# Kernel tuning notes

Hardware: AMD Instinct MI355X
Metric: run time of the kernel (lower is better)

## Reference

```python
import jax, jax.numpy as jnp
import numpy as np

EPS = 1e-5
NH, NP = 12, 4  # heads, points per level


def _ln(x, g, b):
    m = x.mean(-1, keepdims=True)
    v = x.var(-1, keepdims=True)
    return (x - m) / jnp.sqrt(v + EPS) * g + b


def _bilinear(v, g, H_, W_):
    # v: [B, nh, H_*W_, d] flattened feature map; g: [B, nh, Lq, np, 2] normalized locs in [0,1]
    # torch grid_sample(align_corners=False, padding='zeros') with grid = 2*loc-1 => pixel = loc*W - 0.5
    x = g[..., 0] * W_ - 0.5
    y = g[..., 1] * H_ - 0.5
    x0 = jnp.floor(x)
    y0 = jnp.floor(y)
    wx1 = x - x0
    wy1 = y - y0
    wx0 = 1.0 - wx1
    wy0 = 1.0 - wy1
    d = v.shape[-1]
    Bn, nh, Lq, np_ = x.shape
    out = jnp.zeros((Bn, nh, Lq, np_, d), v.dtype)
    for xi, yi, w in ((x0, y0, wx0 * wy0), (x0 + 1, y0, wx1 * wy0),
                      (x0, y0 + 1, wx0 * wy1), (x0 + 1, y0 + 1, wx1 * wy1)):
        valid = (xi >= 0) & (xi < W_) & (yi >= 0) & (yi < H_)
        xc = jnp.clip(xi, 0, W_ - 1).astype(jnp.int32)
        yc = jnp.clip(yi, 0, H_ - 1).astype(jnp.int32)
        idx = (yc * W_ + xc).reshape(Bn, nh, Lq * np_, 1)
        gv = jnp.take_along_axis(v, idx, axis=2).reshape(Bn, nh, Lq, np_, d)
        out = out + (w * valid.astype(v.dtype))[..., None] * gv
    return out


def setup_inputs() -> dict:
    key = jax.random.key(0)
    ks = jax.random.split(key, 16)
    B, Lq, C = 4, 4096, 768
    nl = 1
    Hs = Ws = 64
    Lin = Hs * Ws
    hid = int(C * 0.25)
    s = 0.02
    f32 = jnp.float32
    return {
        'query': jax.random.normal(ks[0], (B, Lq, C), f32),
        'reference_points': jax.random.uniform(ks[1], (B, Lq, nl, 2), f32),
        'feat': jax.random.normal(ks[2], (B, Lin, C), f32),
        'spatial_shapes': np.array([[Hs, Ws]], dtype=np.int64),
        'level_start_index': np.array([0], dtype=np.int64),
        'H': Hs, 'W': Ws,
        'qn_g': jnp.ones(C, f32), 'qn_b': jnp.zeros(C, f32),
        'fn_g': jnp.ones(C, f32), 'fn_b': jnp.zeros(C, f32),
        'Wv': jax.random.normal(ks[3], (C, C), f32) * s, 'bv': jnp.zeros(C, f32),
        'Woff': jax.random.normal(ks[4], (C, NH * nl * NP * 2), f32) * s,
        'boff': jax.random.normal(ks[5], (NH * nl * NP * 2,), f32) * 0.1,
        'Watt': jax.random.normal(ks[6], (C, NH * nl * NP), f32) * s,
        'batt': jnp.zeros(NH * nl * NP, f32),
        'Wout': jax.random.normal(ks[7], (C, C), f32) * s, 'bout': jnp.zeros(C, f32),
        'ffn_g': jnp.ones(C, f32), 'ffn_b': jnp.zeros(C, f32),
        'W1': jax.random.normal(ks[8], (C, hid), f32) * s, 'b1': jnp.zeros(hid, f32),
        'W2': jax.random.normal(ks[9], (hid, C), f32) * s, 'b2': jnp.zeros(C, f32),
    }


def reference(query, reference_points, feat, spatial_shapes, level_start_index, H, W,
              qn_g, qn_b, fn_g, fn_b, Wv, bv, Woff, boff, Watt, batt, Wout, bout,
              ffn_g, ffn_b, W1, b1, W2, b2):
    B, Lq, C = query.shape
    nl = spatial_shapes.shape[0]
    d = C // NH
    qn = _ln(query, qn_g, qn_b)
    fn = _ln(feat, fn_g, fn_b)
    value = (fn @ Wv + bv).reshape(B, -1, NH, d)
    off = (qn @ Woff + boff).reshape(B, Lq, NH, nl, NP, 2)
    attw = jax.nn.softmax((qn @ Watt + batt).reshape(B, Lq, NH, nl * NP), axis=-1)
    attw = attw.reshape(B, Lq, NH, nl, NP)
    # offset normalizer is [W_l, H_l]
    norm = np.stack([spatial_shapes[:, 1], spatial_shapes[:, 0]], -1).astype(np.float32)
    loc = reference_points[:, :, None, :, None, :] + off / jnp.asarray(norm)[None, None, None, :, None, :]
    out = jnp.zeros((B, NH, Lq, d), query.dtype)
    for l in range(nl):
        H_, W_ = int(spatial_shapes[l, 0]), int(spatial_shapes[l, 1])
        s0 = int(level_start_index[l])
        v = value[:, s0:s0 + H_ * W_].transpose(0, 2, 1, 3)       # [B, nh, HW, d]
        g = loc[:, :, :, l].transpose(0, 2, 1, 3, 4)              # [B, nh, Lq, np, 2]
        sampled = _bilinear(v, g, H_, W_)                         # [B, nh, Lq, np, d]
        w = attw[:, :, :, l].transpose(0, 2, 1, 3)                # [B, nh, Lq, np]
        out = out + jnp.sum(sampled * w[..., None], axis=3)
    attn = out.transpose(0, 2, 1, 3).reshape(B, Lq, C) @ Wout + bout
    query = query + attn
    h = _ln(query, ffn_g, ffn_b)
    h = jax.nn.gelu(h @ W1 + b1, approximate=False)
    return query + (h @ W2 + b2)
```

## Files before the change

kernel.cpp:

```cpp
#include <hip/hip_runtime.h>
#include <hip/hip_bf16.h>
#include <math.h>

#define B_    4
#define LQ    4096
#define CC    768
#define NH_   12
#define DH    64
#define NP_   4
#define HH    64
#define WW    64
#define HID   192
#define ROWS  (B_ * LQ)
#define EPS_  1e-5f

typedef __bf16 bf16x8 __attribute__((ext_vector_type(8)));
typedef __bf16 bf16x4 __attribute__((ext_vector_type(4)));
typedef float  f32x4  __attribute__((ext_vector_type(4)));

typedef __attribute__((address_space(3))) void* lds_vp;
typedef const __attribute__((address_space(1))) void* gbl_vp;

__device__ __forceinline__ unsigned pk4_f8(float a, float b, float c, float d) {
    unsigned lo, hi;
    asm volatile("v_cvt_pk_fp8_f32 %0, %1, %2" : "=v"(lo) : "v"(a), "v"(b));
    asm volatile("v_cvt_pk_fp8_f32 %0, %1, %2" : "=v"(hi) : "v"(c), "v"(d));
    return (lo & 0xffffu) | (hi << 16);
}
__device__ __forceinline__ unsigned char to_f8(float a) {
    unsigned r;
    asm volatile("v_cvt_pk_fp8_f32 %0, %1, %1" : "=v"(r) : "v"(a));
    return (unsigned char)r;
}

struct PrepJob { const float* W; unsigned char* Wt; int K; int N; int Npad; };
struct PrepJobs { PrepJob j[6]; };

__inline__ __device__ float wave_sum64(float v) {
    #pragma unroll
    for (int o = 32; o > 0; o >>= 1) v += __shfl_down(v, o, 64);
    return v;
}

__global__ __launch_bounds__(256)
void ln2p_kernel(const float* __restrict__ x0, const float* __restrict__ g0,
                 const float* __restrict__ b0, unsigned char* __restrict__ y0,
                 const float* __restrict__ x1, const float* __restrict__ g1,
                 const float* __restrict__ b1, unsigned char* __restrict__ y1,
                 PrepJobs jobs) {
    __shared__ float tile[64][65];
    __shared__ float red[8];
    int bx = blockIdx.x;
    int t = threadIdx.x;

    if (bx >= 2 * ROWS) {
        int tid = bx - 2 * ROWS;
        PrepJob job = jobs.j[tid / 144];
        int rem = tid % 144;
        int k0 = (rem % 12) * 64, n0 = (rem / 12) * 64;
        if (k0 >= job.K || n0 >= job.Npad) return;
        int c = t & 63, r0 = t >> 6;
        #pragma unroll
        for (int i = 0; i < 16; ++i) {
            int kk = i * 4 + r0;
            float v = 0.f;
            if (k0 + kk < job.K && n0 + c < job.N) v = job.W[(size_t)(k0 + kk) * job.N + n0 + c];
            tile[kk][c] = v;
        }
        __syncthreads();
        #pragma unroll
        for (int i = 0; i < 16; ++i) {
            int nn = i * 4 + r0;
            if (n0 + nn < job.Npad && k0 + c < job.K)
                job.Wt[(size_t)(n0 + nn) * job.K + k0 + c] = to_f8(tile[c][nn] * 64.f);
        }
        return;
    }

    int sel = bx >= ROWS;
    int row = bx - sel * ROWS;
    const float* x = sel ? x1 : x0;
    const float* g = sel ? g1 : g0;
    const float* b = sel ? b1 : b0;
    unsigned char* y = sel ? y1 : y0;
    const float* xr = x + (size_t)row * CC;
    unsigned char* yr = y + (size_t)row * CC;
    f32x4 xv = {0.f, 0.f, 0.f, 0.f};
    if (t < 192) xv = *(const f32x4*)(xr + t * 4);
    float s  = xv[0] + xv[1] + xv[2] + xv[3];
    float s2 = xv[0]*xv[0] + xv[1]*xv[1] + xv[2]*xv[2] + xv[3]*xv[3];
    float ws = wave_sum64(s), ws2 = wave_sum64(s2);
    int w = t >> 6;
    if ((t & 63) == 0) { red[w] = ws; red[4 + w] = ws2; }
    __syncthreads();
    float S  = red[0] + red[1] + red[2] + red[3];
    float S2 = red[4] + red[5] + red[6] + red[7];
    float mean = S / CC;
    float inv  = rsqrtf(S2 / CC - mean * mean + EPS_);
    if (t < 192) {
        f32x4 gv = *(const f32x4*)(g + t * 4);
        f32x4 bv = *(const f32x4*)(b + t * 4);
        float o[4];
        #pragma unroll
        for (int e = 0; e < 4; ++e)
            o[e] = (xv[e] - mean) * inv * gv[e] + bv[e];
        *(unsigned*)(yr + t * 4) = pk4_f8(o[0], o[1], o[2], o[3]);
    }
}

__global__ __launch_bounds__(256)
void ln_bf_kernel(const __bf16* __restrict__ x, const float* __restrict__ g,
                  const float* __restrict__ b, unsigned char* __restrict__ y) {
    int row = blockIdx.x;
    const __bf16* xr = x + (size_t)row * CC;
    unsigned char* yr = y + (size_t)row * CC;
    int t = threadIdx.x;
    float xv[8]; bf16x8 raw = {};
    if (t < 96) raw = *(const bf16x8*)(xr + t * 8);
    float s = 0.f, s2 = 0.f;
    #pragma unroll
    for (int e = 0; e < 8; ++e) { xv[e] = (float)raw[e]; s += xv[e]; s2 += xv[e]*xv[e]; }
    __shared__ float red[8];
    float ws = wave_sum64(s), ws2 = wave_sum64(s2);
    int w = t >> 6;
    if ((t & 63) == 0) { red[w] = ws; red[4 + w] = ws2; }
    __syncthreads();
    float S  = red[0] + red[1] + red[2] + red[3];
    float S2 = red[4] + red[5] + red[6] + red[7];
    float mean = S / CC;
    float inv  = rsqrtf(S2 / CC - mean * mean + EPS_);
    if (t < 96) {
        float o[8];
        #pragma unroll
        for (int e = 0; e < 8; ++e)
            o[e] = (xv[e] - mean) * inv * g[t * 8 + e] + b[t * 8 + e];
        uint2 pk;
        pk.x = pk4_f8(o[0], o[1], o[2], o[3]);
        pk.y = pk4_f8(o[4], o[5], o[6], o[7]);
        *(uint2*)(yr + t * 8) = pk;
    }
}

struct G64Job {
    const unsigned char* A; const unsigned char* Bt;
    const float* ba; const float* bb;
    const void* res; void* out;
    int Nsplit, K, N, flags, nblk, gx;
};

__global__ __launch_bounds__(256, 8)
void gemm64f8(G64Job j0, G64Job j1) {
    __shared__ unsigned char As[3][2048];
    __shared__ unsigned char Bs[3][2048];

    int bid = blockIdx.x;
    G64Job jb = j0;
    if (bid >= j0.nblk) { jb = j1; bid -= j0.nblk; }

    int t = threadIdx.x;
    int lane = t & 63, wave = t >> 6;

    int swz = (bid & 7) * (jb.nblk >> 3) + (bid >> 3);
    int bx = swz % jb.gx, by = swz / jb.gx;
    int bm = by * 64, bn = bx * 64;
    int K = jb.K, N = jb.N;

    f32x4 acc[4] = {};

    int local = t & 127;
    int r = local >> 1, hch = local & 1;
    int sw = (r >> 2) & 1;
    const unsigned char* sbase = (wave < 2)
        ? jb.A  + (size_t)(bm + r) * K + ((hch ^ sw) << 4)
        : jb.Bt + (size_t)(bn + r) * K + ((hch ^ sw) << 4);

    int rsel = lane & 15, kq = lane >> 4;
    int ra = wave * 16 + rsel;
    int aoff = ra * 32 + ((((kq >> 1) ^ ((ra >> 2) & 1)) << 4) | ((kq & 1) << 3));
    int boffs[4];
    #pragma unroll
    for (int j = 0; j < 4; ++j) {
        int n = rsel + j * 16;
        boffs[j] = n * 32 + ((((kq >> 1) ^ ((n >> 2) & 1)) << 4) | ((kq & 1) << 3));
    }

    #define STAGE(bi, kt) do {                                                                    \
        if (wave < 2)                                                                             \
            __builtin_amdgcn_global_load_lds((gbl_vp)(sbase + (kt) * 32),                         \
                (lds_vp)&As[bi][t * 16], 16, 0, 0);                                               \
        else                                                                                      \
            __builtin_amdgcn_global_load_lds((gbl_vp)(sbase + (kt) * 32),                         \
                (lds_vp)&Bs[bi][(t - 128) * 16], 16, 0, 0);                                       \
    } while (0)

    #define COMPUTE(bi) do {                                                                      \
        long afr = *(const long*)&As[bi][aoff];                                                   \
        _Pragma("unroll")                                                                         \
        for (int j = 0; j < 4; ++j) {                                                             \
            long bfr = *(const long*)&Bs[bi][boffs[j]];                                           \
            acc[j] = __builtin_amdgcn_mfma_f32_16x16x32_fp8_fp8(afr, bfr, acc[j], 0, 0, 0);       \
        }                                                                                         \
    } while (0)

    int nt = K >> 5;
    STAGE(0, 0);
    STAGE(1, 1);
    STAGE(2, 2);
    int bi = 0;
    for (int tt = 0; tt < nt; ++tt) {
        if (tt < nt - 2)       asm volatile("s_waitcnt vmcnt(2)\n\ts_barrier" ::: "memory");
        else if (tt == nt - 2) asm volatile("s_waitcnt vmcnt(1)\n\ts_barrier" ::: "memory");
        else                   asm volatile("s_waitcnt vmcnt(0)\n\ts_barrier" ::: "memory");
        COMPUTE(bi);
        asm volatile("s_waitcnt lgkmcnt(0)\n\ts_barrier" ::: "memory");
        if (tt + 3 < nt) STAGE(bi, tt + 3);
        ++bi; if (bi == 3) bi = 0;
    }

    #undef STAGE
    #undef COMPUTE

    int rowq = lane >> 4;
    int do_gelu = jb.flags & 1, out_bf = jb.flags & 2, res_bf = jb.flags & 4, out_f8 = jb.flags & 8;
    const void* res = jb.res;
    #pragma unroll
    for (int j = 0; j < 4; ++j) {
        int c = bn + j * 16 + rsel;
        if (c < N) {
            float bias = (c < jb.Nsplit) ? jb.ba[c] : jb.bb[c - jb.Nsplit];
            #pragma unroll
            for (int r4 = 0; r4 < 4; ++r4) {
                int m = bm + wave * 16 + rowq * 4 + r4;
                float v = acc[j][r4] * 0.015625f + bias;
                if (do_gelu) v = 0.5f * v * (1.f + erff(v * 0.70710678118f));
                size_t oi = (size_t)m * N + c;
                if (res) v += res_bf ? (float)((const __bf16*)res)[oi]
                                     : ((const float*)res)[oi];
                if (out_f8)      ((unsigned char*)jb.out)[oi] = to_f8(v);
                else if (out_bf) ((__bf16*)jb.out)[oi] = (__bf16)v;
                else             ((float*)jb.out)[oi]  = v;
            }
        }
    }
}

__global__ __launch_bounds__(256)
void sample_kernel(const __bf16* __restrict__ value, const float* __restrict__ offatt,
                   const float* __restrict__ refp, unsigned char* __restrict__ out) {
    int wid  = blockIdx.x * 4 + (threadIdx.x >> 6);
    int lane = threadIdx.x & 63;
    int h  = wid % NH_;
    int bq = wid / NH_;
    int b  = bq / LQ;

    const float* oa = offatt + (size_t)bq * 144;
    float rx = refp[(size_t)bq * 2 + 0] * (float)WW - 0.5f;
    float ry = refp[(size_t)bq * 2 + 1] * (float)HH - 0.5f;

    float l0 = oa[96 + h * 4 + 0], l1 = oa[96 + h * 4 + 1];
    float l2 = oa[96 + h * 4 + 2], l3 = oa[96 + h * 4 + 3];
    float mx = fmaxf(fmaxf(l0, l1), fmaxf(l2, l3));
    float e0 = __expf(l0 - mx), e1 = __expf(l1 - mx);
    float e2 = __expf(l2 - mx), e3 = __expf(l3 - mx);
    float rs = 1.f / (e0 + e1 + e2 + e3);

    int pp = lane >> 4;
    int g  = lane & 15;
    float wpl = (pp == 0) ? e0 : (pp == 1) ? e1 : (pp == 2) ? e2 : e3;
    wpl *= rs;

    const float* oxy = oa + h * 8 + pp * 2;
    float x = rx + oxy[0];
    float y = ry + oxy[1];
    float x0f = floorf(x), y0f = floorf(y);
    float wx1 = x - x0f, wy1 = y - y0f;
    float wx0 = 1.f - wx1, wy0 = 1.f - wy1;
    int x0 = (int)x0f, y0 = (int)y0f;
    int x1 = x0 + 1, y1 = y0 + 1;
    float mx0 = ((unsigned)x0 < (unsigned)WW) ? wx0 : 0.f;
    float mx1 = ((unsigned)x1 < (unsigned)WW) ? wx1 : 0.f;
    float my0 = (((unsigned)y0 < (unsigned)HH) ? wy0 : 0.f) * wpl;
    float my1 = (((unsigned)y1 < (unsigned)HH) ? wy1 : 0.f) * wpl;
    int xc0 = x0 & (WW - 1), xc1 = x1 & (WW - 1);
    int r0 = (y0 & (HH - 1)) << 6, r1 = (y1 & (HH - 1)) << 6;

    const __bf16* vbase = value + (size_t)b * (LQ * CC) + h * DH + g * 4;
    bf16x4 v00 = *(const bf16x4*)(vbase + (size_t)(r0 + xc0) * CC);
    bf16x4 v01 = *(const bf16x4*)(vbase + (size_t)(r0 + xc1) * CC);
    bf16x4 v10 = *(const bf16x4*)(vbase + (size_t)(r1 + xc0) * CC);
    bf16x4 v11 = *(const bf16x4*)(vbase + (size_t)(r1 + xc1) * CC);
    float w00 = mx0 * my0, w01 = mx1 * my0, w10 = mx0 * my1, w11 = mx1 * my1;

    f32x4 acc;
    #pragma unroll
    for (int e = 0; e < 4; ++e)
        acc[e] = w00 * (float)v00[e] + w01 * (float)v01[e]
               + w10 * (float)v10[e] + w11 * (float)v11[e];

    #pragma unroll
    for (int e = 0; e < 4; ++e) {
        acc[e] += __shfl_xor(acc[e], 16, 64);
        acc[e] += __shfl_xor(acc[e], 32, 64);
    }
    if (pp == 0) {
        *(unsigned*)(out + (size_t)bq * CC + h * DH + g * 4) =
            pk4_f8(acc[0], acc[1], acc[2], acc[3]);
    }
}

extern "C" void kernel_launch(void* const* d_in, const int* in_sizes, int n_in,
                              void* d_out, int out_size, void* d_ws, size_t ws_size,
                              hipStream_t stream) {
    const float* query = (const float*)d_in[0];
    const float* refp  = (const float*)d_in[1];
    const float* feat  = (const float*)d_in[2];
    const float* qn_g  = (const float*)d_in[7];
    const float* qn_b  = (const float*)d_in[8];
    const float* fn_g  = (const float*)d_in[9];
    const float* fn_b  = (const float*)d_in[10];
    const float* Wv    = (const float*)d_in[11];
    const float* bv    = (const float*)d_in[12];
    const float* Woff  = (const float*)d_in[13];
    const float* boff  = (const float*)d_in[14];
    const float* Watt  = (const float*)d_in[15];
    const float* batt  = (const float*)d_in[16];
    const float* Wout  = (const float*)d_in[17];
    const float* bout  = (const float*)d_in[18];
    const float* ffn_g = (const float*)d_in[19];
    const float* ffn_b = (const float*)d_in[20];
    const float* W1    = (const float*)d_in[21];
    const float* b1    = (const float*)d_in[22];
    const float* W2    = (const float*)d_in[23];
    const float* b2    = (const float*)d_in[24];
    float* out = (float*)d_out;

    char* ws = (char*)d_ws;
    unsigned char* Wv8    = (unsigned char*)(ws + 0);
    unsigned char* Wcomb8 = (unsigned char*)(ws + 1179648);
    unsigned char* Wout8  = (unsigned char*)(ws + 1572864);
    unsigned char* W18    = (unsigned char*)(ws + 2752512);
    unsigned char* W28    = (unsigned char*)(ws + 3145728);
    float*  offatt_f = (float*)(ws + 3670016);
    unsigned char* h1_f8 = (unsigned char*)offatt_f;
    __bf16* value_bf = (__bf16*)(ws + 13107200);
    unsigned char* fn_f8   = (unsigned char*)(ws + 38273024);
    unsigned char* samp_f8 = fn_f8;
    unsigned char* qn_f8   = (unsigned char*)(ws + 50855936);
    unsigned char* h_f8    = qn_f8;
    __bf16* attn_bf  = (__bf16*)(ws + 63438848);

    dim3 blk(256);

    PrepJobs jobs;
    jobs.j[0] = {Wv,   Wv8,             768, 768, 768};
    jobs.j[1] = {Woff, Wcomb8,          768,  96,  96};
    jobs.j[2] = {Watt, Wcomb8 + 96*768, 768,  48,  96};
    jobs.j[3] = {Wout, Wout8,           768, 768, 768};
    jobs.j[4] = {W1,   W18,             768, 192, 192};
    jobs.j[5] = {W2,   W28,             192, 768, 768};
    ln2p_kernel<<<2 * ROWS + 864, blk, 0, stream>>>(query, qn_g, qn_b, qn_f8,
                                                    feat,  fn_g, fn_b, fn_f8, jobs);

    G64Job joff = {qn_f8, Wcomb8, boff, batt, nullptr, offatt_f,
                   96, CC, 144, 0, 768, 3};
    G64Job jval = {fn_f8, Wv8, bv, bv, nullptr, value_bf,
                   CC, CC, CC, 2, 3072, 12};
    gemm64f8<<<768 + 3072, blk, 0, stream>>>(joff, jval);

    sample_kernel<<<ROWS * NH_ / 4, blk, 0, stream>>>(value_bf, offatt_f, refp, samp_f8);

    G64Job jout5 = {samp_f8, Wout8, bout, bout, query, attn_bf,
                    CC, CC, CC, 2, 3072, 12};
    gemm64f8<<<3072, blk, 0, stream>>>(jout5, jout5);

    ln_bf_kernel<<<ROWS, blk, 0, stream>>>(attn_bf, ffn_g, ffn_b, h_f8);

    G64Job jw1 = {h_f8, W18, b1, b1, nullptr, h1_f8,
                  HID, CC, HID, 1 | 8, 768, 3};
    gemm64f8<<<768, blk, 0, stream>>>(jw1, jw1);

    G64Job jw2 = {h1_f8, W28, b2, b2, attn_bf, out,
                  CC, HID, CC, 4, 3072, 12};
    gemm64f8<<<3072, blk, 0, stream>>>(jw2, jw2);
}
```

Measured before the change: 408.5 us.

## Double K-tile depth in fp8 GEMM and issue prefetch before compute

The fp8 64x64 GEMM now loads 64-wide K tiles instead of 32-wide, with all 256 threads loading both A and B, and a 2-bit XOR swizzle in LDS. The pipeline prefetches two tiles ahead into a rotating 3-buffer ring and issues the next load before the MFMA work. This removes the second per-iteration barrier and halves the loop trip count. In exchange LDS use doubles and launch bounds drop to 6 blocks per CU, which lowers occupancy.

```diff
diff --git a/kernel.cpp b/kernel.cpp
--- a/kernel.cpp
+++ b/kernel.cpp
@@ -148,10 +148,10 @@
     int Nsplit, K, N, flags, nblk, gx;
 };
 
-__global__ __launch_bounds__(256, 8)
+__global__ __launch_bounds__(256, 6)
 void gemm64f8(G64Job j0, G64Job j1) {
-    __shared__ unsigned char As[3][2048];
-    __shared__ unsigned char Bs[3][2048];
+    __shared__ unsigned char As[3][4096];
+    __shared__ unsigned char Bs[3][4096];
 
     int bid = blockIdx.x;
     G64Job jb = j0;
@@ -167,53 +167,57 @@
 
     f32x4 acc[4] = {};
 
-    int local = t & 127;
-    int r = local >> 1, hch = local & 1;
-    int sw = (r >> 2) & 1;
-    const unsigned char* sbase = (wave < 2)
-        ? jb.A  + (size_t)(bm + r) * K + ((hch ^ sw) << 4)
-        : jb.Bt + (size_t)(bn + r) * K + ((hch ^ sw) << 4);
+    int r = t >> 2, cp = t & 3;
+    int gc = cp ^ ((r >> 2) & 3);
+    const unsigned char* aS = jb.A  + (size_t)(bm + r) * K + gc * 16;
+    const unsigned char* bS = jb.Bt + (size_t)(bn + r) * K + gc * 16;
 
     int rsel = lane & 15, kq = lane >> 4;
     int ra = wave * 16 + rsel;
-    int aoff = ra * 32 + ((((kq >> 1) ^ ((ra >> 2) & 1)) << 4) | ((kq & 1) << 3));
-    int boffs[4];
-    #pragma unroll
-    for (int j = 0; j < 4; ++j) {
-        int n = rsel + j * 16;
-        boffs[j] = n * 32 + ((((kq >> 1) ^ ((n >> 2) & 1)) << 4) | ((kq & 1) << 3));
+    int aoff[2], boff[4][2];
+    #pragma unroll
+    for (int h = 0; h < 2; ++h) {
+        int ch = ((h << 1) | (kq >> 1)) ^ ((ra >> 2) & 3);
+        aoff[h] = ra * 64 + ch * 16 + (kq & 1) * 8;
+        #pragma unroll
+        for (int j = 0; j < 4; ++j) {
+            int n = rsel + j * 16;
+            int cb = ((h << 1) | (kq >> 1)) ^ ((n >> 2) & 3);
+            boff[j][h] = n * 64 + cb * 16 + (kq & 1) * 8;
+        }
     }
 
     #define STAGE(bi, kt) do {                                                                    \
-        if (wave < 2)                                                                             \
-            __builtin_amdgcn_global_load_lds((gbl_vp)(sbase + (kt) * 32),                         \
-                (lds_vp)&As[bi][t * 16], 16, 0, 0);                                               \
-        else                                                                                      \
-            __builtin_amdgcn_global_load_lds((gbl_vp)(sbase + (kt) * 32),                         \
-                (lds_vp)&Bs[bi][(t - 128) * 16], 16, 0, 0);                                       \
+        __builtin_amdgcn_global_load_lds((gbl_vp)(aS + (kt) * 64),                                \
+            (lds_vp)&As[bi][t * 16], 16, 0, 0);                                                   \
+        __builtin_amdgcn_global_load_lds((gbl_vp)(bS + (kt) * 64),                                \
+            (lds_vp)&Bs[bi][t * 16], 16, 0, 0);                                                   \
     } while (0)
 
     #define COMPUTE(bi) do {                                                                      \
-        long afr = *(const long*)&As[bi][aoff];                                                   \
         _Pragma("unroll")                                                                         \
-        for (int j = 0; j < 4; ++j) {                                                             \
-            long bfr = *(const long*)&Bs[bi][boffs[j]];                                           \
-            acc[j] = __builtin_amdgcn_mfma_f32_16x16x32_fp8_fp8(afr, bfr, acc[j], 0, 0, 0);       \
+        for (int h = 0; h < 2; ++h) {                                                             \
+            long afr = *(const long*)&As[bi][aoff[h]];                                            \
+            _Pragma("unroll")                                                                     \
+            for (int j = 0; j < 4; ++j) {                                                         \
+                long bfr = *(const long*)&Bs[bi][boff[j][h]];                                     \
+                acc[j] = __builtin_amdgcn_mfma_f32_16x16x32_fp8_fp8(afr, bfr, acc[j], 0, 0, 0);   \
+            }                                                                                     \
         }                                                                                         \
     } while (0)
 
-    int nt = K >> 5;
+    int nt = K >> 6;
     STAGE(0, 0);
     STAGE(1, 1);
-    STAGE(2, 2);
     int bi = 0;
     for (int tt = 0; tt < nt; ++tt) {
-        if (tt < nt - 2)       asm volatile("s_waitcnt vmcnt(2)\n\ts_barrier" ::: "memory");
-        else if (tt == nt - 2) asm volatile("s_waitcnt vmcnt(1)\n\ts_barrier" ::: "memory");
-        else                   asm volatile("s_waitcnt vmcnt(0)\n\ts_barrier" ::: "memory");
+        if (tt < nt - 1) asm volatile("s_waitcnt vmcnt(2)\n\ts_barrier" ::: "memory");
+        else             asm volatile("s_waitcnt vmcnt(0)\n\ts_barrier" ::: "memory");
+        if (tt + 2 < nt) {
+            int nb = bi + 2; if (nb >= 3) nb -= 3;
+            STAGE(nb, tt + 2);
+        }
         COMPUTE(bi);
-        asm volatile("s_waitcnt lgkmcnt(0)\n\ts_barrier" ::: "memory");
-        if (tt + 3 < nt) STAGE(bi, tt + 3);
         ++bi; if (bi == 3) bi = 0;
     }
 
```

Result: faster. 374.5 us (-8.3%).
